# Kernel tuning notes

Hardware: AMD Instinct MI355X
Metric: run time of the kernel (lower is better)

Reference implementation:

```python
import jax, jax.numpy as jnp
import numpy as np

INV_SQRT2 = 0.7071067811865476
N, E, K, S = 10000, 120000, 8, 7
DE, DA, DT, DR, DC = 128, 128, 64, 16, 16
T = E * K

def act(x):
    return jax.nn.silu(x)

def residual_stack(x, Ws):
    # Ws: (n_layers, 2, D, D); GemNet ResidualLayer: two Dense+act, scaled skip
    for lw in Ws:
        y = act(act(x @ lw[0]) @ lw[1])
        x = (x + y) * INV_SQRT2
    return x

def bilinear(rbf_W1, sph, m, id_reduce, id_ragged, W):
    # EfficientInteractionBilinear (GemNet): ragged scatter into (E,Kmax,emb) then basis contractions
    m2 = jnp.zeros((rbf_W1.shape[0], sph.shape[1], m.shape[-1]), m.dtype)
    m2 = m2.at[id_reduce, id_ragged].set(m)          # (E, K, DT)
    sum_k = jnp.einsum('eks,ekc->esc', sph, m2)      # (E, S, DT)
    a = jnp.einsum('ejs,esc->ejc', rbf_W1, sum_k)    # (E, DC, DT)
    return jnp.einsum('ejc,cju->eu', a, W)           # (E, DT)

def _forward(h, m_st, rbf_h, rbf3, cbf_rbfW1, cbf_sph,
             W_mlp_st, W_m_kt, W_t_rbf, W_down, W_bil, W_st3, W_ts3,
             res_before, res_after, W_ae_rbf, W_ae_in, res_atom, W_asi, res_m,
             idx_s, idx_t, idx_swap, id3_kt, id3_st, id3_ragged_idx):
    x_skip = m_st @ W_mlp_st
    # --- TripletInteraction ---
    m_kt = act(m_st @ W_m_kt)
    m_kt = m_kt * (rbf3 @ W_t_rbf)        # scale_rbf == 1.0 (identity ScaleFactor)
    m_kt = act(m_kt @ W_down)             # (E, DT)
    xb = bilinear(cbf_rbfW1, cbf_sph, m_kt[id3_kt], id3_st, id3_ragged_idx, W_bil)
    x_st = act(xb @ W_st3)
    x_ts = act(xb @ W_ts3)[idx_swap]
    x3 = (x_st + x_ts) * INV_SQRT2
    # --- merge + residual stacks ---
    x = (x_skip + x3) * INV_SQRT2
    x = residual_stack(x, res_before)
    x = (x + m_st) * INV_SQRT2
    x = residual_stack(x, res_after)
    # --- AtomEmbedding: edge->atom scatter-add ---
    xa = x * (rbf_h @ W_ae_rbf)
    h2 = jax.ops.segment_sum(xa, idx_t, num_segments=h.shape[0])  # scale_sum == 1.0
    h_new = residual_stack(act(h2 @ W_ae_in), res_atom)
    # --- AtomSelfInteraction: gather-concat-Dense ---
    m = act(jnp.concatenate([h_new[idx_s], h_new[idx_t], x], axis=-1) @ W_asi)
    m = residual_stack(m, res_m)
    m = (m + x) * INV_SQRT2
    return h_new, m

def setup_inputs():
    key = jax.random.key(0)
    ks = jax.random.split(key, 24)
    def w(k, shape):
        return jax.random.normal(k, shape, jnp.float32) * (1.0 / np.sqrt(shape[-2]))
    return dict(
        h=jax.random.normal(ks[0], (N, DA), jnp.float32),
        m_st=jax.random.normal(ks[1], (E, DE), jnp.float32),
        rbf_h=jax.random.uniform(ks[2], (E, DR), jnp.float32),
        rbf3=jax.random.uniform(ks[3], (E, DR), jnp.float32),
        cbf_rbfW1=jax.random.normal(ks[4], (E, DC, S), jnp.float32) * 0.2,
        cbf_sph=jax.random.normal(ks[5], (E, K, S), jnp.float32) * 0.2,
        W_mlp_st=w(ks[6], (DE, DE)),
        W_m_kt=w(ks[7], (DE, DE)),
        W_t_rbf=w(ks[8], (DR, DE)),
        W_down=w(ks[9], (DE, DT)),
        W_bil=jax.random.normal(ks[10], (DT, DC, DT), jnp.float32) * (1.0 / np.sqrt(DT * DC)),
        W_st3=w(ks[11], (DT, DE)),
        W_ts3=w(ks[12], (DT, DE)),
        res_before=w(ks[13], (1, 2, DE, DE)),
        res_after=w(ks[14], (2, 2, DE, DE)),
        W_ae_rbf=w(ks[15], (DR, DE)),
        W_ae_in=w(ks[16], (DE, DA)),
        res_atom=w(ks[17], (2, 2, DA, DA)),
        W_asi=w(ks[18], (2 * DA + DE, DE)),
        res_m=w(ks[19], (2, 2, DE, DE)),
        idx_s=jax.random.randint(ks[20], (E,), 0, N, jnp.int32),
        idx_t=jax.random.randint(ks[21], (E,), 0, N, jnp.int32),
        idx_swap=jax.random.permutation(ks[22], E).astype(jnp.int32),
        id3_kt=jax.random.randint(ks[23], (T,), 0, E, jnp.int32),
        id3_st=jnp.repeat(jnp.arange(E, dtype=jnp.int32), K),
        id3_ragged_idx=jnp.tile(jnp.arange(K, dtype=jnp.int32), E),
    )

def reference(h, m_st, rbf_h, rbf3, cbf_rbfW1, cbf_sph,
              W_mlp_st, W_m_kt, W_t_rbf, W_down, W_bil, W_st3, W_ts3,
              res_before, res_after, W_ae_rbf, W_ae_in, res_atom, W_asi, res_m,
              idx_s, idx_t, idx_swap, id3_kt, id3_st, id3_ragged_idx):
    return _forward(h, m_st, rbf_h, rbf3, cbf_rbfW1, cbf_sph,
                    W_mlp_st, W_m_kt, W_t_rbf, W_down, W_bil, W_st3, W_ts3,
                    res_before, res_after, W_ae_rbf, W_ae_in, res_atom, W_asi, res_m,
                    idx_s, idx_t, idx_swap, id3_kt, id3_st, id3_ragged_idx)
```

## Files before the change

kernel.cpp:

```cpp
#include <hip/hip_runtime.h>


#define EE 120000
#define NA 10000

constexpr float C_INV = 0.70710678118654752440f;

using f32x4 = __attribute__((ext_vector_type(4))) float;
using f32x2 = __attribute__((ext_vector_type(2))) float;
using s16x8 = __attribute__((ext_vector_type(8))) short;
using s16x4 = __attribute__((ext_vector_type(4))) short;

__device__ __forceinline__ float act_silu(float x) { return x / (1.0f + __expf(-x)); }

__device__ __forceinline__ unsigned short f2bf(float f) {
    unsigned int u = __float_as_uint(f);
    u += 0x7fffu + ((u >> 16) & 1u);
    return (unsigned short)(u >> 16);
}
__device__ __forceinline__ float bf2f(unsigned short h) {
    return __uint_as_float(((unsigned int)h) << 16);
}
__device__ __forceinline__ unsigned int cvtpk(float a, float b) {
    unsigned int r;
    asm("v_cvt_pk_bf16_f32 %0, %1, %2" : "=v"(r) : "v"(a), "v"(b));
    return r;
}

template<int MT, int KQ>
__device__ __forceinline__ void load_w(const unsigned short* __restrict__ W, int KW,
                                       int l, s16x8 (&a)[MT][KQ])
{
    const int fr = l & 15;
    const int k8 = (l >> 4) << 3;
    #pragma unroll
    for (int mt = 0; mt < MT; ++mt)
        #pragma unroll
        for (int kq = 0; kq < KQ; ++kq)
            a[mt][kq] = *(const s16x8*)&W[(size_t)(mt * 16 + fr) * KW + kq * 32 + k8];
}

template<int MT, int NF, int KQ>
__device__ __forceinline__ void gemm_pre(
    const s16x8 (&a)[MT][KQ], const char* ldsB, int RS,
    int rowBase, int l, f32x4 (&acc)[MT][NF])
{
    const int fr = l & 15;
    const int k8 = (l >> 4) << 3;
    #pragma unroll
    for (int kq = 0; kq < KQ; ++kq) {
        s16x8 b[NF];
        #pragma unroll
        for (int nf = 0; nf < NF; ++nf) {
            const int row = rowBase + nf * 16 + fr;
            const int kb  = ((kq * 32 + k8) * 2) ^ ((row & 7) << 4);
            b[nf] = *(const s16x8*)(ldsB + row * RS + kb);
        }
        #pragma unroll
        for (int mt = 0; mt < MT; ++mt)
            #pragma unroll
            for (int nf = 0; nf < NF; ++nf)
                acc[mt][nf] = __builtin_amdgcn_mfma_f32_16x16x32_bf16(
                    a[mt][kq], b[nf], acc[mt][nf], 0, 0, 0);
    }
}

template<int MT, int NF>
__device__ __forceinline__ void zacc(f32x4 (&acc)[MT][NF])
{
    #pragma unroll
    for (int mt = 0; mt < MT; ++mt)
        #pragma unroll
        for (int nf = 0; nf < NF; ++nf)
            acc[mt][nf] = (f32x4){0.f, 0.f, 0.f, 0.f};
}

__device__ __forceinline__ void packA(char* lds, int RS, int row, int outF0, f32x4 v)
{
    uint2 p;
    p.x = cvtpk(v[0], v[1]);
    p.y = cvtpk(v[2], v[3]);
    *(uint2*)(lds + row * RS + ((outF0 * 2) ^ ((row & 7) << 4))) = p;
}

__device__ __forceinline__ void store_bf4(unsigned short* dst, f32x4 v)
{
    uint2 p;
    p.x = cvtpk(v[0], v[1]);
    p.y = cvtpk(v[2], v[3]);
    *(uint2*)dst = p;
}

template<int ROWS>
__device__ __forceinline__ void stage_f32(char* lds, const float* __restrict__ src,
                                          int row0, int M, int tid)
{
    #pragma unroll
    for (int u = 0; u < ROWS * 16 / 512; ++u) {
        const int flat = tid + u * 512;
        const int row  = flat >> 4;
        const int k8   = (flat & 15) << 3;
        const int grow = row0 + row;
        uint4 val = {0u, 0u, 0u, 0u};
        if (grow < M) {
            const float* p = src + (size_t)grow * 128 + k8;
            f32x4 lo = *(const f32x4*)p;
            f32x4 hi = *(const f32x4*)(p + 4);
            val.x = cvtpk(lo[0], lo[1]);
            val.y = cvtpk(lo[2], lo[3]);
            val.z = cvtpk(hi[0], hi[1]);
            val.w = cvtpk(hi[2], hi[3]);
        }
        *(uint4*)(lds + row * 256 + ((k8 * 2) ^ ((row & 7) << 4))) = val;
    }
}

template<bool MSTM, int NF>
__device__ __forceinline__ void res_layer(
    char* A, char* B,
    const unsigned short* W0, const unsigned short* W1,
    int wm, int wn, int l, f32x4 (&x)[2][NF],
    const s16x4 (*ms)[NF])
{
    const int fr = l & 15;
    const int fq = (l >> 4) << 2;

    s16x8 aw[2][4];
    load_w<2, 4>(W0 + (size_t)(wm * 32) * 128, 128, l, aw);
    f32x4 acc[2][NF];
    zacc(acc);
    gemm_pre<2, NF, 4>(aw, A, 256, wn * NF * 16, l, acc);

    s16x8 aw1[2][4];
    load_w<2, 4>(W1 + (size_t)(wm * 32) * 128, 128, l, aw1);

    #pragma unroll
    for (int mt = 0; mt < 2; ++mt)
        #pragma unroll
        for (int nf = 0; nf < NF; ++nf) {
            const int row = wn * NF * 16 + nf * 16 + fr;
            const int of0 = wm * 32 + mt * 16 + fq;
            f32x4 v;
            #pragma unroll
            for (int q = 0; q < 4; ++q) v[q] = act_silu(acc[mt][nf][q]);
            packA(B, 256, row, of0, v);
        }
    __syncthreads();

    zacc(acc);
    gemm_pre<2, NF, 4>(aw1, B, 256, wn * NF * 16, l, acc);
    #pragma unroll
    for (int mt = 0; mt < 2; ++mt)
        #pragma unroll
        for (int nf = 0; nf < NF; ++nf) {
            const int row = wn * NF * 16 + nf * 16 + fr;
            const int of0 = wm * 32 + mt * 16 + fq;
            #pragma unroll
            for (int q = 0; q < 4; ++q)
                x[mt][nf][q] = (x[mt][nf][q] + act_silu(acc[mt][nf][q])) * C_INV;
            if (MSTM) {
                #pragma unroll
                for (int q = 0; q < 4; ++q)
                    x[mt][nf][q] = (x[mt][nf][q] +
                                    bf2f((unsigned short)ms[mt][nf][q])) * C_INV;
            }
            packA(A, 256, row, of0, x[mt][nf]);
        }
    __syncthreads();
}

__device__ __forceinline__ s16x4 read_frag(const char* lds, int row, int of0)
{
    return *(const s16x4*)(lds + row * 256 + ((of0 * 2) ^ ((row & 7) << 4)));
}

__global__ __launch_bounds__(512, 4) void front_k(
    const float* __restrict__ m_st, const float* __restrict__ rbf3,
    const float* __restrict__ Wtrbf,
    const unsigned short* __restrict__ Wmkt, const unsigned short* __restrict__ Wdown,
    unsigned short* __restrict__ mkt_b)
{
    __shared__ char A[128 * 256];
    __shared__ float Wt[16 * 128];
    __shared__ float R3[128 * 17];
    const int tid = threadIdx.x;
    const int l = tid & 63, w = tid >> 6, wm = w & 3, wn = w >> 2;
    const int fr = l & 15, fq = (l >> 4) << 2;
    const int row0 = blockIdx.x * 128;

    s16x8 aw[2][4];
    load_w<2, 4>(Wmkt + (size_t)(wm * 32) * 128, 128, l, aw);

    for (int u = tid; u < 2048; u += 512) Wt[u] = Wtrbf[u];
    for (int u = tid; u < 2048; u += 512) {
        const int row = u >> 4, k = u & 15;
        const int grow = row0 + row;
        R3[row * 17 + k] = (grow < EE) ? rbf3[(size_t)grow * 16 + k] : 0.f;
    }

    stage_f32<128>(A, m_st, row0, EE, tid);
    __syncthreads();

    f32x4 acc[2][4];
    zacc(acc);
    gemm_pre<2, 4, 4>(aw, A, 256, wn * 64, l, acc);

    s16x8 aw2[1][4];
    load_w<1, 4>(Wdown + (size_t)(wm * 16) * 128, 128, l, aw2);

    __syncthreads();
    #pragma unroll
    for (int mt = 0; mt < 2; ++mt)
        #pragma unroll
        for (int nf = 0; nf < 4; ++nf) {
            const int row = wn * 64 + nf * 16 + fr;
            const int grow = row0 + row;
            const int of0 = wm * 32 + mt * 16 + fq;
            f32x4 v = {0.f, 0.f, 0.f, 0.f};
            if (grow < EE) {
                f32x4 sc = {0.f, 0.f, 0.f, 0.f};
                #pragma unroll
                for (int k = 0; k < 16; ++k) {
                    const float r = R3[row * 17 + k];
                    f32x4 wv = *(const f32x4*)&Wt[k * 128 + of0];
                    sc += r * wv;
                }
                #pragma unroll
                for (int q = 0; q < 4; ++q)
                    v[q] = act_silu(acc[mt][nf][q]) * sc[q];
            }
            packA(A, 256, row, of0, v);
        }
    __syncthreads();

    f32x4 acc2[1][4];
    zacc(acc2);
    gemm_pre<1, 4, 4>(aw2, A, 256, wn * 64, l, acc2);
    #pragma unroll
    for (int nf = 0; nf < 4; ++nf) {
        const int row = wn * 64 + nf * 16 + fr;
        const int grow = row0 + row;
        if (grow >= EE) continue;
        const int of0 = wm * 16 + fq;
        f32x4 v;
        #pragma unroll
        for (int q = 0; q < 4; ++q) v[q] = act_silu(acc2[0][nf][q]);
        store_bf4(&mkt_b[(size_t)grow * 64 + of0], v);
    }
}

__global__ __launch_bounds__(512, 4) void chain_k(
    const float* __restrict__ m_st,
    const unsigned short* __restrict__ yst, const unsigned short* __restrict__ yts,
    const int* __restrict__ idx_swap,
    const unsigned short* __restrict__ Wmlp,
    const unsigned short* __restrict__ Wrb0, const unsigned short* __restrict__ Wrb1,
    const unsigned short* __restrict__ Wra0, const unsigned short* __restrict__ Wra1,
    const unsigned short* __restrict__ Wra2, const unsigned short* __restrict__ Wra3,
    unsigned short* __restrict__ xb_out)
{
    __shared__ char A[128 * 256];
    __shared__ char B[128 * 256];
    const int tid = threadIdx.x;
    const int l = tid & 63, w = tid >> 6, wm = w & 3, wn = w >> 2;
    const int fr = l & 15, fq = (l >> 4) << 2;
    const int row0 = blockIdx.x * 128;

    s16x8 aw[2][4];
    load_w<2, 4>(Wmlp + (size_t)(wm * 32) * 128, 128, l, aw);

    stage_f32<128>(A, m_st, row0, EE, tid);
    __syncthreads();

    f32x4 acc[2][4];
    zacc(acc);
    gemm_pre<2, 4, 4>(aw, A, 256, wn * 64, l, acc);

    s16x4 ms[2][4];
    #pragma unroll
    for (int mt = 0; mt < 2; ++mt)
        #pragma unroll
        for (int nf = 0; nf < 4; ++nf)
            ms[mt][nf] = read_frag(A, wn * 64 + nf * 16 + fr, wm * 32 + mt * 16 + fq);

    f32x4 x[2][4];
    #pragma unroll
    for (int mt = 0; mt < 2; ++mt)
        #pragma unroll
        for (int nf = 0; nf < 4; ++nf) {
            const int row = wn * 64 + nf * 16 + fr;
            const int grow = row0 + row;
            const int of0 = wm * 32 + mt * 16 + fq;
            if (grow < EE) {
                s16x4 a = *(const s16x4*)&yst[(size_t)grow * 128 + of0];
                const int sw = idx_swap[grow];
                s16x4 b = *(const s16x4*)&yts[(size_t)sw * 128 + of0];
                #pragma unroll
                for (int q = 0; q < 4; ++q)
                    x[mt][nf][q] = (acc[mt][nf][q] +
                        (bf2f((unsigned short)a[q]) + bf2f((unsigned short)b[q])) * C_INV) * C_INV;
            } else {
                x[mt][nf] = (f32x4){0.f, 0.f, 0.f, 0.f};
            }
        }
    __syncthreads();
    #pragma unroll
    for (int mt = 0; mt < 2; ++mt)
        #pragma unroll
        for (int nf = 0; nf < 4; ++nf)
            packA(A, 256, wn * 64 + nf * 16 + fr, wm * 32 + mt * 16 + fq, x[mt][nf]);
    __syncthreads();

    res_layer<true , 4>(A, B, Wrb0, Wrb1, wm, wn, l, x, ms);
    res_layer<false, 4>(A, B, Wra0, Wra1, wm, wn, l, x, nullptr);
    res_layer<false, 4>(A, B, Wra2, Wra3, wm, wn, l, x, nullptr);

    #pragma unroll
    for (int mt = 0; mt < 2; ++mt)
        #pragma unroll
        for (int nf = 0; nf < 4; ++nf) {
            const int row = wn * 64 + nf * 16 + fr;
            const int grow = row0 + row;
            if (grow >= EE) continue;
            const int of0 = wm * 32 + mt * 16 + fq;
            store_bf4(&xb_out[(size_t)grow * 128 + of0], x[mt][nf]);
        }
}

__global__ __launch_bounds__(512, 4) void atom_k(
    const float* __restrict__ h2,
    const unsigned short* __restrict__ Wae,
    const unsigned short* __restrict__ Wr0, const unsigned short* __restrict__ Wr1,
    const unsigned short* __restrict__ Wr2, const unsigned short* __restrict__ Wr3,
    float* __restrict__ out_h, unsigned short* __restrict__ h_b)
{
    __shared__ char A[64 * 256];
    __shared__ char B[64 * 256];
    const int tid = threadIdx.x;
    const int l = tid & 63, w = tid >> 6, wm = w & 3, wn = w >> 2;
    const int fr = l & 15, fq = (l >> 4) << 2;
    const int row0 = blockIdx.x * 64;

    s16x8 aw[2][4];
    load_w<2, 4>(Wae + (size_t)(wm * 32) * 128, 128, l, aw);

    #pragma unroll
    for (int u = 0; u < 2; ++u) {
        const int flat = tid + u * 512;
        const int row  = flat >> 4;
        const int k8   = (flat & 15) << 3;
        const int grow = row0 + row;
        uint4 val = {0u, 0u, 0u, 0u};
        if (grow < NA) {
            const float* p = h2 + (size_t)grow * 128 + k8;
            f32x4 lo = *(const f32x4*)p;
            f32x4 hi = *(const f32x4*)(p + 4);
            val.x = cvtpk(lo[0], lo[1]);
            val.y = cvtpk(lo[2], lo[3]);
            val.z = cvtpk(hi[0], hi[1]);
            val.w = cvtpk(hi[2], hi[3]);
        }
        *(uint4*)(A + row * 256 + ((k8 * 2) ^ ((row & 7) << 4))) = val;
    }
    __syncthreads();

    f32x4 acc[2][2];
    zacc(acc);
    gemm_pre<2, 2, 4>(aw, A, 256, wn * 32, l, acc);
    f32x4 x[2][2];
    #pragma unroll
    for (int mt = 0; mt < 2; ++mt)
        #pragma unroll
        for (int nf = 0; nf < 2; ++nf)
            #pragma unroll
            for (int q = 0; q < 4; ++q)
                x[mt][nf][q] = act_silu(acc[mt][nf][q]);
    __syncthreads();
    #pragma unroll
    for (int mt = 0; mt < 2; ++mt)
        #pragma unroll
        for (int nf = 0; nf < 2; ++nf)
            packA(A, 256, wn * 32 + nf * 16 + fr, wm * 32 + mt * 16 + fq, x[mt][nf]);
    __syncthreads();

    res_layer<false, 2>(A, B, Wr0, Wr1, wm, wn, l, x, nullptr);
    res_layer<false, 2>(A, B, Wr2, Wr3, wm, wn, l, x, nullptr);

    #pragma unroll
    for (int mt = 0; mt < 2; ++mt)
        #pragma unroll
        for (int nf = 0; nf < 2; ++nf) {
            const int row = wn * 32 + nf * 16 + fr;
            const int grow = row0 + row;
            if (grow >= NA) continue;
            const int of0 = wm * 32 + mt * 16 + fq;
            *(f32x4*)&out_h[(size_t)grow * 128 + of0] = x[mt][nf];
            store_bf4(&h_b[(size_t)grow * 128 + of0], x[mt][nf]);
        }
}

__global__ __launch_bounds__(512, 4) void asi_k(
    const unsigned short* __restrict__ h_b, const unsigned short* __restrict__ x_b,
    const int* __restrict__ idx_s, const int* __restrict__ idx_t,
    const unsigned short* __restrict__ Wasi,
    const unsigned short* __restrict__ Wm0, const unsigned short* __restrict__ Wm1,
    const unsigned short* __restrict__ Wm2, const unsigned short* __restrict__ Wm3,
    float* __restrict__ out_m)
{
    __shared__ char A[128 * 256];
    __shared__ char B[128 * 256];
    const int tid = threadIdx.x;
    const int l = tid & 63, w = tid >> 6, wm = w & 3, wn = w >> 2;
    const int fr = l & 15, fq = (l >> 4) << 2;
    const int row0 = blockIdx.x * 128;

    f32x4 acc[2][4];
    zacc(acc);

    for (int c = 0; c < 3; ++c) {
        s16x8 aw[2][4];
        load_w<2, 4>(Wasi + (size_t)(wm * 32) * 384 + c * 128, 384, l, aw);
        #pragma unroll
        for (int u = 0; u < 4; ++u) {
            const int flat = tid + u * 512;
            const int row = flat >> 4;
            const int k8 = (flat & 15) << 3;
            const int grow = row0 + row;
            s16x8 v = {0, 0, 0, 0, 0, 0, 0, 0};
            if (grow < EE) {
                const unsigned short* src =
                    (c == 0) ? h_b + (size_t)idx_s[grow] * 128
                  : (c == 1) ? h_b + (size_t)idx_t[grow] * 128
                             : x_b + (size_t)grow * 128;
                v = *(const s16x8*)&src[k8];
            }
            *(s16x8*)(A + row * 256 + ((k8 * 2) ^ ((row & 7) << 4))) = v;
        }
        __syncthreads();
        gemm_pre<2, 4, 4>(aw, A, 256, wn * 64, l, acc);
        __syncthreads();
    }

    f32x4 x[2][4];
    #pragma unroll
    for (int mt = 0; mt < 2; ++mt)
        #pragma unroll
        for (int nf = 0; nf < 4; ++nf)
            #pragma unroll
            for (int q = 0; q < 4; ++q)
                x[mt][nf][q] = act_silu(acc[mt][nf][q]);
    #pragma unroll
    for (int mt = 0; mt < 2; ++mt)
        #pragma unroll
        for (int nf = 0; nf < 4; ++nf)
            packA(A, 256, wn * 64 + nf * 16 + fr, wm * 32 + mt * 16 + fq, x[mt][nf]);
    __syncthreads();

    res_layer<false, 4>(A, B, Wm0, Wm1, wm, wn, l, x, nullptr);
    res_layer<false, 4>(A, B, Wm2, Wm3, wm, wn, l, x, nullptr);

    #pragma unroll
    for (int mt = 0; mt < 2; ++mt)
        #pragma unroll
        for (int nf = 0; nf < 4; ++nf) {
            const int row = wn * 64 + nf * 16 + fr;
            const int grow = row0 + row;
            if (grow >= EE) continue;
            const int of0 = wm * 32 + mt * 16 + fq;
            s16x4 xv = *(const s16x4*)&x_b[(size_t)grow * 128 + of0];
            f32x4 o;
            #pragma unroll
            for (int q = 0; q < 4; ++q)
                o[q] = (x[mt][nf][q] + bf2f((unsigned short)xv[q])) * C_INV;
            *(f32x4*)&out_m[(size_t)grow * 128 + of0] = o;
        }
}

__global__ void hist_k(const int* __restrict__ idxt, int* __restrict__ cnt)
{
    int i = blockIdx.x * 256 + threadIdx.x;
    if (i < EE) atomicAdd(&cnt[idxt[i]], 1);
}

__global__ __launch_bounds__(256) void scan_k(const int* __restrict__ cnt,
                                              int* __restrict__ start, int* __restrict__ wrk)
{
    __shared__ int ps[256];
    const int t = threadIdx.x;
    int s = 0;
    for (int j = 0; j < 40; ++j) {
        int idx = t * 40 + j;
        if (idx < NA) s += cnt[idx];
    }
    ps[t] = s;
    __syncthreads();
    for (int off = 1; off < 256; off <<= 1) {
        int v = (t >= off) ? ps[t - off] : 0;
        __syncthreads();
        ps[t] += v;
        __syncthreads();
    }
    int run = ps[t] - s;
    for (int j = 0; j < 40; ++j) {
        int idx = t * 40 + j;
        if (idx < NA) {
            start[idx] = run;
            wrk[idx] = run;
            run += cnt[idx];
        }
    }
    if (t == 255) start[NA] = ps[255];
}

__global__ void place_k(const int* __restrict__ idxt, int* __restrict__ wrk,
                        int* __restrict__ order)
{
    int i = blockIdx.x * 256 + threadIdx.x;
    if (i < EE) {
        int pos = atomicAdd(&wrk[idxt[i]], 1);
        order[pos] = i;
    }
}

__global__ __launch_bounds__(256) void segsum_k(
    const unsigned short* __restrict__ x_b, const float* __restrict__ rbf_h,
    const float* __restrict__ Wae, const int* __restrict__ start,
    const int* __restrict__ order, float* __restrict__ h2)
{
    const int tid = threadIdx.x;
    const int l = tid & 63, w = tid >> 6;
    const int a = blockIdx.x * 4 + w;
    if (a >= NA) return;

    float wc[32];
    #pragma unroll
    for (int j = 0; j < 16; ++j) {
        f32x2 v = *(const f32x2*)(Wae + j * 128 + 2 * l);
        wc[2 * j] = v[0]; wc[2 * j + 1] = v[1];
    }

    const int s = start[a], e_end = start[a + 1];
    float acc0 = 0.f, acc1 = 0.f;
    for (int i = s; i < e_end; ++i) {
        const int e = __builtin_amdgcn_readfirstlane(order[i]);
        const unsigned int xv = *(const unsigned int*)(x_b + (size_t)e * 128 + 2 * l);
        const float* rp = rbf_h + (size_t)e * 16;
        float c0 = 0.f, c1 = 0.f;
        #pragma unroll
        for (int j = 0; j < 16; ++j) {
            float r = rp[j];
            c0 += r * wc[2 * j];
            c1 += r * wc[2 * j + 1];
        }
        acc0 += bf2f((unsigned short)(xv & 0xffff)) * c0;
        acc1 += bf2f((unsigned short)(xv >> 16)) * c1;
    }
    f32x2 o; o[0] = acc0; o[1] = acc1;
    *(f32x2*)&h2[(size_t)a * 128 + 2 * l] = o;
}

__global__ void wconv_k(const float* __restrict__ Wbil, unsigned short* __restrict__ WT)
{
    int t = blockIdx.x * 256 + threadIdx.x;
    int u = t >> 10, k = t & 1023, j = k >> 6, c = k & 63;
    WT[t] = f2bf(Wbil[(size_t)(c * 16 + j) * 64 + u]);
}

struct WDesc { const float* src; int K; int N; int off; };
struct WTab  { WDesc d[21]; };

__global__ void wconvall_k(WTab tab, unsigned short* __restrict__ dst)
{
    WDesc d = tab.d[blockIdx.x];
    const int tot = d.K * d.N;
    for (int i = threadIdx.x; i < tot; i += 256) {
        int n = i / d.K, k = i - n * d.K;
        dst[d.off + i] = f2bf(d.src[(size_t)k * d.N + n]);
    }
}

__global__ __launch_bounds__(512) void bilinear8_k(
    const unsigned short* __restrict__ mkt,
    const float* __restrict__ rbfW1,
    const float* __restrict__ sph,
    const int*   __restrict__ id3kt,
    const unsigned short* __restrict__ WT,
    const unsigned short* __restrict__ Wst3,
    const unsigned short* __restrict__ Wts3,
    unsigned short* __restrict__ yst,
    unsigned short* __restrict__ yts)
{
    __shared__ unsigned short aS[32 * 1024];
    __shared__ float Cs[32 * 128];
    float* pS = (float*)aS;
    float* sphS = (float*)(aS + 16384);
    float* rbS  = sphS + 32 * 56;

    const int tid = threadIdx.x;
    const int l   = tid & 63;
    const int w   = tid >> 6;
    const int e0  = blockIdx.x * 32;
    const int fr  = l & 15;
    const int fq  = (l >> 4) << 2;

    {
        const f32x4* sg = (const f32x4*)(sph + (size_t)e0 * 56);
        for (int u = tid; u < 448; u += 512) ((f32x4*)sphS)[u] = sg[u];
        const f32x4* rg = (const f32x4*)(rbfW1 + (size_t)e0 * 112);
        for (int u = tid; u < 896; u += 512) ((f32x4*)rbS)[u] = rg[u];
    }

    int ids[4][8];
    #pragma unroll
    for (int r = 0; r < 4; ++r) {
        const int eG = e0 + r * 8 + w;
        #pragma unroll
        for (int k = 0; k < 8; ++k) ids[r][k] = id3kt[eG * 8 + k];
    }
    unsigned int m0[8], m1[8], m2v[8], m3[8];
    #pragma unroll
    for (int k = 0; k < 8; ++k) m0[k] = mkt[(size_t)ids[0][k] * 64 + l];
    #pragma unroll
    for (int k = 0; k < 8; ++k) m1[k] = mkt[(size_t)ids[1][k] * 64 + l];
    #pragma unroll
    for (int k = 0; k < 8; ++k) m2v[k] = mkt[(size_t)ids[2][k] * 64 + l];
    #pragma unroll
    for (int k = 0; k < 8; ++k) m3[k] = mkt[(size_t)ids[3][k] * 64 + l];

    __syncthreads();

    {
        const int e = tid >> 4;
        const int j = tid & 15;
        float rb[7];
        #pragma unroll
        for (int s = 0; s < 7; ++s) rb[s] = rbS[e * 112 + j * 7 + s];
        float cr[8];
        #pragma unroll
        for (int k = 0; k < 8; ++k) {
            float a = 0.f;
            #pragma unroll
            for (int s = 0; s < 7; ++s)
                a += rb[s] * sphS[e * 56 + k * 7 + s];
            cr[k] = a;
        }
        f32x4 lo = {cr[0], cr[1], cr[2], cr[3]};
        f32x4 hi = {cr[4], cr[5], cr[6], cr[7]};
        *(f32x4*)&Cs[e * 128 + j * 8]     = lo;
        *(f32x4*)&Cs[e * 128 + j * 8 + 4] = hi;
    }
    __syncthreads();

    #pragma unroll
    for (int r = 0; r < 4; ++r) {
        const int eL = r * 8 + w;
        const float* Ce = &Cs[eL * 128];
        const unsigned int* mm = (r == 0) ? m0 : (r == 1) ? m1 : (r == 2) ? m2v : m3;
        float mv[8];
        #pragma unroll
        for (int k = 0; k < 8; ++k) mv[k] = __uint_as_float(mm[k] << 16);
        unsigned short* arow = aS + eL * 1024;
        const int lsw = l ^ ((eL & 7) << 3);
        #pragma unroll
        for (int j = 0; j < 16; ++j) {
            f32x4 c0 = *(const f32x4*)&Ce[j * 8];
            f32x4 c1 = *(const f32x4*)&Ce[j * 8 + 4];
            float av = c0[0] * mv[0] + c0[1] * mv[1] + c0[2] * mv[2] + c0[3] * mv[3]
                     + c1[0] * mv[4] + c1[1] * mv[5] + c1[2] * mv[6] + c1[3] * mv[7];
            arow[j * 64 + lsw] = f2bf(av);
        }
    }

    s16x8 bfrag[4][4];
    {
        const int u  = l & 15;
        const int kh = w * 128 + ((l >> 4) << 3);
        #pragma unroll
        for (int nt = 0; nt < 4; ++nt)
            #pragma unroll
            for (int kq = 0; kq < 4; ++kq)
                bfrag[nt][kq] = *(const s16x8*)&WT[(size_t)(nt * 16 + u) * 1024 + kh + kq * 32];
    }
    __syncthreads();

    f32x4 acc[2][4];
    #pragma unroll
    for (int mt = 0; mt < 2; ++mt)
        #pragma unroll
        for (int nt = 0; nt < 4; ++nt)
            acc[mt][nt] = (f32x4){0.f, 0.f, 0.f, 0.f};

    const int kbase = w * 128 + ((l >> 4) << 3);
    #pragma unroll
    for (int kq = 0; kq < 4; ++kq) {
        s16x8 afr[2];
        #pragma unroll
        for (int mt = 0; mt < 2; ++mt) {
            const int row = mt * 16 + (l & 15);
            const int kk  = (kbase + kq * 32) ^ ((row & 7) << 3);
            afr[mt] = *(const s16x8*)&aS[row * 1024 + kk];
        }
        #pragma unroll
        for (int mt = 0; mt < 2; ++mt)
            #pragma unroll
            for (int nt = 0; nt < 4; ++nt)
                acc[mt][nt] = __builtin_amdgcn_mfma_f32_16x16x32_bf16(
                    afr[mt], bfrag[nt][kq], acc[mt][nt], 0, 0, 0);
    }
    __syncthreads();

    #pragma unroll
    for (int mt = 0; mt < 2; ++mt)
        #pragma unroll
        for (int nt = 0; nt < 4; ++nt)
            #pragma unroll
            for (int q = 0; q < 4; ++q) {
                const int e = mt * 16 + ((l >> 4) << 2) + q;
                const int u = nt * 16 + (l & 15);
                pS[(w * 32 + e) * 64 + u] = acc[mt][nt][q];
            }
    __syncthreads();

    f32x4 s;
    {
        const int e  = tid >> 4;
        const int u0 = (tid & 15) << 2;
        s = (f32x4){0.f, 0.f, 0.f, 0.f};
        #pragma unroll
        for (int ww = 0; ww < 8; ++ww)
            s += *(const f32x4*)&pS[(ww * 32 + e) * 64 + u0];
    }
    __syncthreads();

    unsigned short* xbS = aS;
    {
        const int e  = tid >> 4;
        const int u0 = (tid & 15) << 2;
        uint2 p;
        p.x = cvtpk(s[0], s[1]);
        p.y = cvtpk(s[2], s[3]);
        *(uint2*)((char*)xbS + e * 128 + ((u0 * 2) ^ ((e & 7) << 4))) = p;
    }
    __syncthreads();

    const unsigned short* Wsel = (w < 4) ? Wst3 : Wts3;
    unsigned short*       ysel = (w < 4) ? yst : yts;
    const int wmF = w & 3;

    s16x8 awF[2][2];
    load_w<2, 2>(Wsel + (size_t)(wmF * 32) * 64, 64, l, awF);
    f32x4 accF[2][2];
    zacc(accF);
    gemm_pre<2, 2, 2>(awF, (const char*)xbS, 128, 0, l, accF);

    #pragma unroll
    for (int mt = 0; mt < 2; ++mt)
        #pragma unroll
        for (int nf = 0; nf < 2; ++nf) {
            const int row = nf * 16 + fr;
            const int of0 = wmF * 32 + mt * 16 + fq;
            f32x4 v;
            #pragma unroll
            for (int q = 0; q < 4; ++q) v[q] = act_silu(accF[mt][nf][q]);
            store_bf4(&ysel[(size_t)(e0 + row) * 128 + of0], v);
        }
}

extern "C" void kernel_launch(void* const* d_in, const int* in_sizes, int n_in,
                              void* d_out, int out_size, void* d_ws, size_t ws_size,
                              hipStream_t stream)
{
    const float* m_st      = (const float*)d_in[1];
    const float* rbf_h     = (const float*)d_in[2];
    const float* rbf3      = (const float*)d_in[3];
    const float* cbf_rbfW1 = (const float*)d_in[4];
    const float* cbf_sph   = (const float*)d_in[5];
    const float* W_mlp_st  = (const float*)d_in[6];
    const float* W_m_kt    = (const float*)d_in[7];
    const float* W_t_rbf   = (const float*)d_in[8];
    const float* W_down    = (const float*)d_in[9];
    const float* W_bil     = (const float*)d_in[10];
    const float* W_st3     = (const float*)d_in[11];
    const float* W_ts3     = (const float*)d_in[12];
    const float* resb      = (const float*)d_in[13];
    const float* resa      = (const float*)d_in[14];
    const float* W_ae_rbf  = (const float*)d_in[15];
    const float* W_ae_in   = (const float*)d_in[16];
    const float* resat     = (const float*)d_in[17];
    const float* W_asi     = (const float*)d_in[18];
    const float* resm      = (const float*)d_in[19];
    const int*   idx_s     = (const int*)d_in[20];
    const int*   idx_t     = (const int*)d_in[21];
    const int*   idx_swap  = (const int*)d_in[22];
    const int*   id3_kt    = (const int*)d_in[23];

    float* h2 = (float*)d_ws;
    unsigned short* yst_b   = (unsigned short*)(h2 + (size_t)NA * 128);
    unsigned short* yts_b   = yst_b + (size_t)EE * 128;
    unsigned short* x_b     = yts_b + (size_t)EE * 128;
    unsigned short* mkt_b   = x_b + (size_t)EE * 128;
    unsigned short* xb_b    = mkt_b + (size_t)EE * 64;
    unsigned short* h_b     = xb_b + (size_t)EE * 64;
    unsigned short* WTbil   = h_b + (size_t)NA * 128;
    unsigned short* WTall   = WTbil + 65536;
    int* cnt   = (int*)(WTall + 352256);
    int* start = cnt + NA;
    int* wrk   = start + NA + 1;
    int* order = wrk + NA;

    float* out_h = (float*)d_out;
    float* out_m = out_h + (size_t)NA * 128;

    const dim3 blk(256);
    const dim3 blk5(512);
    const int gE  = (EE + 127) / 128;
    const int gN64 = (NA + 63) / 64;
    constexpr size_t SQ = 128 * 128;

    WTab tab; int off = 0; int oi = 0;
    auto put = [&](const float* s, int K, int N) {
        int o = off; tab.d[oi].src = s; tab.d[oi].K = K; tab.d[oi].N = N;
        tab.d[oi].off = o; ++oi; off += K * N; return o;
    };
    const int o_mlp  = put(W_mlp_st, 128, 128);
    const int o_mktw = put(W_m_kt, 128, 128);
    const int o_down = put(W_down, 128, 64);
    const int o_st3  = put(W_st3, 64, 128);
    const int o_ts3  = put(W_ts3, 64, 128);
    const int o_rb0  = put(resb, 128, 128);
    const int o_rb1  = put(resb + SQ, 128, 128);
    const int o_ra0  = put(resa, 128, 128);
    const int o_ra1  = put(resa + SQ, 128, 128);
    const int o_ra2  = put(resa + 2 * SQ, 128, 128);
    const int o_ra3  = put(resa + 3 * SQ, 128, 128);
    const int o_aein = put(W_ae_in, 128, 128);
    const int o_rat0 = put(resat, 128, 128);
    const int o_rat1 = put(resat + SQ, 128, 128);
    const int o_rat2 = put(resat + 2 * SQ, 128, 128);
    const int o_rat3 = put(resat + 3 * SQ, 128, 128);
    const int o_asi  = put(W_asi, 384, 128);
    const int o_rm0  = put(resm, 128, 128);
    const int o_rm1  = put(resm + SQ, 128, 128);
    const int o_rm2  = put(resm + 2 * SQ, 128, 128);
    const int o_rm3  = put(resm + 3 * SQ, 128, 128);

    hipMemsetAsync(cnt, 0, NA * sizeof(int), stream);
    wconv_k<<<65536 / 256, blk, 0, stream>>>(W_bil, WTbil);
    wconvall_k<<<21, blk, 0, stream>>>(tab, WTall);
    hist_k<<<(EE + 255) / 256, blk, 0, stream>>>(idx_t, cnt);
    scan_k<<<1, blk, 0, stream>>>(cnt, start, wrk);
    place_k<<<(EE + 255) / 256, blk, 0, stream>>>(idx_t, wrk, order);

    front_k<<<gE, blk5, 0, stream>>>(m_st, rbf3, W_t_rbf,
                                     WTall + o_mktw, WTall + o_down, mkt_b);
    bilinear8_k<<<EE / 32, blk5, 0, stream>>>(
        mkt_b, cbf_rbfW1, cbf_sph, id3_kt, WTbil,
        WTall + o_st3, WTall + o_ts3, yst_b, yts_b);
    chain_k<<<gE, blk5, 0, stream>>>(
        m_st, yst_b, yts_b, idx_swap,
        WTall + o_mlp, WTall + o_rb0, WTall + o_rb1,
        WTall + o_ra0, WTall + o_ra1, WTall + o_ra2, WTall + o_ra3,
        x_b);
    segsum_k<<<(NA + 3) / 4, blk, 0, stream>>>(x_b, rbf_h, W_ae_rbf, start, order, h2);
    atom_k<<<gN64, blk5, 0, stream>>>(
        h2, WTall + o_aein,
        WTall + o_rat0, WTall + o_rat1, WTall + o_rat2, WTall + o_rat3,
        out_h, h_b);
    asi_k<<<gE, blk5, 0, stream>>>(
        h_b, x_b, idx_s, idx_t,
        WTall + o_asi,
        WTall + o_rm0, WTall + o_rm1, WTall + o_rm2, WTall + o_rm3,
        out_m);
}
```

Before: 603.7 us.

## Coalesce chain output stores, split segsum across two waves, swizzle bilinear LDS

The chain kernel's final output is now written by copying the already-packed swizzled LDS tile row-wise with 16-byte stores, instead of scattered 8-byte stores from MFMA fragments. segsum now gives each atom two waves that take alternate edges and combine their partial sums through shared memory, doubling parallelism per atom. The bilinear kernel XOR-swizzles its partial-sum LDS layout to reduce bank conflicts. Risks: the chain store depends on A holding the final x after the last residual layer, and segsum has an early return ahead of __syncthreads.

```diff
diff --git a/kernel.cpp b/kernel.cpp
--- a/kernel.cpp
+++ b/kernel.cpp
@@ -316,15 +316,16 @@
     res_layer<false, 4>(A, B, Wra2, Wra3, wm, wn, l, x, nullptr);
 
     #pragma unroll
-    for (int mt = 0; mt < 2; ++mt)
-        #pragma unroll
-        for (int nf = 0; nf < 4; ++nf) {
-            const int row = wn * 64 + nf * 16 + fr;
-            const int grow = row0 + row;
-            if (grow >= EE) continue;
-            const int of0 = wm * 32 + mt * 16 + fq;
-            store_bf4(&xb_out[(size_t)grow * 128 + of0], x[mt][nf]);
-        }
+    for (int u = 0; u < 4; ++u) {
+        const int flat = tid + u * 512;
+        const int row  = flat >> 4;
+        const int k8   = (flat & 15) << 3;
+        const int grow = row0 + row;
+        if (grow < EE) {
+            uint4 v = *(const uint4*)(A + row * 256 + ((k8 * 2) ^ ((row & 7) << 4)));
+            *(uint4*)&xb_out[(size_t)grow * 128 + k8] = v;
+        }
+    }
 }
 
 __global__ __launch_bounds__(512, 4) void atom_k(
@@ -527,9 +528,12 @@
     const float* __restrict__ Wae, const int* __restrict__ start,
     const int* __restrict__ order, float* __restrict__ h2)
 {
+    __shared__ float part[2][128];
     const int tid = threadIdx.x;
     const int l = tid & 63, w = tid >> 6;
-    const int a = blockIdx.x * 4 + w;
+    const int ai = w >> 1;
+    const int half = w & 1;
+    const int a = blockIdx.x * 2 + ai;
     if (a >= NA) return;
 
     float wc[32];
@@ -541,7 +545,7 @@
 
     const int s = start[a], e_end = start[a + 1];
     float acc0 = 0.f, acc1 = 0.f;
-    for (int i = s; i < e_end; ++i) {
+    for (int i = s + half; i < e_end; i += 2) {
         const int e = __builtin_amdgcn_readfirstlane(order[i]);
         const unsigned int xv = *(const unsigned int*)(x_b + (size_t)e * 128 + 2 * l);
         const float* rp = rbf_h + (size_t)e * 16;
@@ -555,8 +559,17 @@
         acc0 += bf2f((unsigned short)(xv & 0xffff)) * c0;
         acc1 += bf2f((unsigned short)(xv >> 16)) * c1;
     }
-    f32x2 o; o[0] = acc0; o[1] = acc1;
-    *(f32x2*)&h2[(size_t)a * 128 + 2 * l] = o;
+    if (half == 1) {
+        part[ai][2 * l]     = acc0;
+        part[ai][2 * l + 1] = acc1;
+    }
+    __syncthreads();
+    if (half == 0) {
+        f32x2 o;
+        o[0] = acc0 + part[ai][2 * l];
+        o[1] = acc1 + part[ai][2 * l + 1];
+        *(f32x2*)&h2[(size_t)a * 128 + 2 * l] = o;
+    }
 }
 
 __global__ void wconv_k(const float* __restrict__ Wbil, unsigned short* __restrict__ WT)
@@ -579,7 +592,7 @@
     }
 }
 
-__global__ __launch_bounds__(512) void bilinear8_k(
+__global__ __launch_bounds__(512) void bilinear9_k(
     const unsigned short* __restrict__ mkt,
     const float* __restrict__ rbfW1,
     const float* __restrict__ sph,
@@ -717,14 +730,14 @@
             for (int q = 0; q < 4; ++q) {
                 const int e = mt * 16 + ((l >> 4) << 2) + q;
                 const int u = nt * 16 + (l & 15);
-                pS[(w * 32 + e) * 64 + u] = acc[mt][nt][q];
+                pS[(w * 32 + e) * 64 + (u ^ ((e & 3) << 4))] = acc[mt][nt][q];
             }
     __syncthreads();
 
     f32x4 s;
     {
         const int e  = tid >> 4;
-        const int u0 = (tid & 15) << 2;
+        const int u0 = ((tid & 15) << 2) ^ ((e & 3) << 4);
         s = (f32x4){0.f, 0.f, 0.f, 0.f};
         #pragma unroll
         for (int ww = 0; ww < 8; ++ww)
@@ -735,7 +748,7 @@
     unsigned short* xbS = aS;
     {
         const int e  = tid >> 4;
-        const int u0 = (tid & 15) << 2;
+        const int u0 = ((tid & 15) << 2) ^ ((e & 3) << 4);
         uint2 p;
         p.x = cvtpk(s[0], s[1]);
         p.y = cvtpk(s[2], s[3]);
@@ -853,7 +866,7 @@
 
     front_k<<<gE, blk5, 0, stream>>>(m_st, rbf3, W_t_rbf,
                                      WTall + o_mktw, WTall + o_down, mkt_b);
-    bilinear8_k<<<EE / 32, blk5, 0, stream>>>(
+    bilinear9_k<<<EE / 32, blk5, 0, stream>>>(
         mkt_b, cbf_rbfW1, cbf_sph, id3_kt, WTbil,
         WTall + o_st3, WTall + o_ts3, yst_b, yts_b);
     chain_k<<<gE, blk5, 0, stream>>>(
@@ -861,7 +874,7 @@
         WTall + o_mlp, WTall + o_rb0, WTall + o_rb1,
         WTall + o_ra0, WTall + o_ra1, WTall + o_ra2, WTall + o_ra3,
         x_b);
-    segsum_k<<<(NA + 3) / 4, blk, 0, stream>>>(x_b, rbf_h, W_ae_rbf, start, order, h2);
+    segsum_k<<<(NA + 1) / 2, blk, 0, stream>>>(x_b, rbf_h, W_ae_rbf, start, order, h2);
     atom_k<<<gN64, blk5, 0, stream>>>(
         h2, WTall + o_aein,
         WTall + o_rat0, WTall + o_rat1, WTall + o_rat2, WTall + o_rat3,
```

Result: no change. 595.2 us (-1.4%).
